# Kernel tuning notes

Hardware: AMD Instinct MI355X
Metric: run time of the kernel (lower is better)

## Reference

```python
import jax, jax.numpy as jnp
import numpy as np

HDIM = 1024
CDIM = 256
TEMPER = 10.0
IGNORE_OUT = 0.0
EPS = 1e-6


def setup_inputs() -> dict:
    key = jax.random.key(0)
    ks = jax.random.split(key, 6)
    B, T, D = 2, 128, 384
    x = jax.random.normal(ks[0], (B, T, D), jnp.float32)
    y = jax.random.normal(ks[1], (B, T, D), jnp.float32)
    # xavier-normal style init for the two linear layers
    W_enc = jax.random.normal(ks[2], (D, HDIM), jnp.float32) * np.sqrt(2.0 / (D + HDIM))
    b_enc = jnp.zeros((HDIM,), jnp.float32)
    W_dec = jax.random.normal(ks[3], (HDIM, D), jnp.float32) * np.sqrt(2.0 / (D + HDIM))
    b_dec = jnp.zeros((D,), jnp.float32)
    return {"x": x, "y": y, "W_enc": W_enc, "b_enc": b_enc, "W_dec": W_dec, "b_dec": b_dec}


def reference(x, y, W_enc, b_enc, W_dec, b_dec):
    B, T, D = x.shape
    n_iter = HDIM // CDIM
    pad = D - 1
    # shift_idx[s, j] = s + j : window of width D at offset s, s in [0, 2D-2]
    shift_idx = jnp.arange(2 * D - 1)[:, None] + jnp.arange(D)[None, :]

    seq_mask = (y == IGNORE_OUT)                       # (B,T,D) bool
    denom_seq = jnp.sum(~seq_mask).astype(x.dtype)
    qn = jnp.linalg.norm(y, axis=-1)                   # (B,T)

    mask_prev = None
    x_dis, losses = [], []
    for _ in range(n_iter):
        # --- _pad_for_shift: (B,T,2D-1,D) shifted windows of x ---
        kp = jnp.pad(x, ((0, 0), (0, 0), (pad, pad)))  # (B,T,3D-2)
        kpt = kp[..., shift_idx]                       # (B,T,2D-1,D)
        # --- _score (cos) + argmax over shifts ---
        kn = jnp.linalg.norm(kpt, axis=-1)             # (B,T,2D-1)
        sim = jnp.einsum('btsd,btd->bts', kpt, y) / (qn[..., None] * kn + EPS)
        sim = jnp.where(jnp.isnan(sim), 0.0, sim)
        theta = jnp.argmax(sim, axis=-1)               # (B,T) int
        x_opt = jnp.take_along_axis(kpt, theta[..., None, None], axis=-2)[..., 0, :]  # (B,T,D)
        # --- attention: elementwise cos-scaled score, temp softmax, detached ---
        dn = (jnp.linalg.norm(x_opt, axis=-1, keepdims=True)
              * jnp.linalg.norm(y, axis=-1, keepdims=True) + EPS)
        attn = jax.nn.softmax((x_opt * y / dn) / TEMPER, axis=-1)
        attn = jnp.where(jnp.isnan(attn), 0.0, attn)
        attn = jax.lax.stop_gradient(attn)
        x_attn = x_opt * attn
        # --- _reverse_pad_for_shift: window at offset 2D-2-theta ---
        kp2 = jnp.pad(x_attn, ((0, 0), (0, 0), (pad, pad)))
        rev_idx = (2 * D - 2 - theta)[..., None] + jnp.arange(D)  # (B,T,D)
        x_ele = jnp.take_along_axis(kp2, rev_idx, axis=-1)         # (B,T,D)
        # --- self_net: encoder -> top-k sparsify -> decoder_self ---
        h = x_ele @ W_enc + b_enc                      # (B,T,HDIM)
        if mask_prev is not None:
            h = jnp.where(mask_prev > 0, 1e-10, h)
        _, idx_top = jax.lax.top_k(h, CDIM)            # (B,T,CDIM)
        flat = idx_top.reshape(B * T, CDIM)
        mask_cur = jnp.zeros((B * T, HDIM), x.dtype).at[
            jnp.arange(B * T)[:, None], flat].set(1.0).reshape(B, T, HDIM)
        if mask_prev is None:
            mask_prev = mask_cur
        else:
            mask_prev = mask_prev + mask_cur - mask_prev * mask_cur
        h = h * mask_cur
        out = h @ W_dec + b_dec                        # (B,T,D)
        x_dis.append(out)
        # --- SeqLoss (masked MSE, mean-reduced by count of valid elems) ---
        err = jnp.where(seq_mask, 0.0, (out - x) ** 2) / denom_seq
        losses.append(jnp.sum(err))
    return jnp.stack(x_dis), jnp.stack(losses)
```

## Files before the change

### kernel.cpp

```cpp
#include <hip/hip_runtime.h>
#include <math.h>

#define DD 384
#define HD 1024
#define CD 256
#define NS 765
#define NITER 4
#define NROWS 256
#define TEMPER_F 10.0f
#define EPSF 1e-6f
#define CUTF 1e-10f

typedef unsigned long long u64;
typedef unsigned int u32;

__device__ __forceinline__ u32 flipf(float f) {
    u32 u = __float_as_uint(f);
    return u ^ ((u32)((int)u >> 31) | 0x80000000u);
}
__device__ __forceinline__ float unflipf(u32 s) {
    u32 fl = ~s;
    u32 u = (fl & 0x80000000u) ? (fl ^ 0x80000000u) : ~fl;
    return __uint_as_float(u);
}
__device__ __forceinline__ u64 shflx64(u64 v, int m) {
    int lo = __shfl_xor((int)(u32)v, m, 64);
    int hi = __shfl_xor((int)(u32)(v >> 32), m, 64);
    return ((u64)(u32)hi << 32) | (u32)lo;
}

__global__ __launch_bounds__(512) void fused_kernel(
    const float* __restrict__ x, const float* __restrict__ y,
    const float* __restrict__ Wenc, const float* __restrict__ benc,
    const float* __restrict__ Wdec, const float* __restrict__ bdec,
    float* __restrict__ out_xdis, float* __restrict__ lossp,
    int* __restrict__ ycnt)
{
    const int row  = blockIdx.x;
    const int tid  = threadIdx.x;
    const int lane = tid & 63;
    const int wid  = tid >> 6;

    __shared__ __align__(16) float xpad[1152];
    __shared__ __align__(16) float yr[DD];
    __shared__ float xa[DD];
    __shared__ __align__(16) float xe_s[DD];
    __shared__ __align__(16) float hpart[HD];
    __shared__ __align__(16) u64   skey[HD];
    __shared__ __align__(16) uint2 dec2[HD];
    __shared__ float wred[8];
    __shared__ int   wredi[8];
    __shared__ float wredn[8];
    __shared__ float s_sc[4];
    __shared__ int   s_theta, s_fb;
    __shared__ float loss4[NITER];

    const float* xrow = x + row * DD;
    const float* yrow = y + row * DD;

    for (int i = tid; i < 1152; i += 512)
        xpad[i] = (i >= DD - 1 && i < 2 * DD - 1) ? xrow[i - (DD - 1)] : 0.f;
    if (tid < DD) yr[tid] = yrow[tid];
    __syncthreads();

    if (tid < DD) {
        float p = yr[tid] * yr[tid];
        for (int o = 32; o; o >>= 1) p += __shfl_xor(p, o, 64);
        if (lane == 0) wred[wid] = p;
    }
    __syncthreads();
    if (tid == 0) {
        float s = 0.f;
        for (int w = 0; w < 6; ++w) s += wred[w];
        s_sc[0] = sqrtf(s);
    }
    __syncthreads();
    const float qn = s_sc[0];

    float bv = -INFINITY; int bs = 0x7fffffff; float bn = 0.f;
    if (tid < 192) {
        const float4* xp4 = (const float4*)xpad;
        const float4* yp4 = (const float4*)yr;
        float4 A = xp4[tid];
        const float f0 = A.x * A.x, f1 = A.y * A.y, f2 = A.z * A.z;
        float d0 = 0.f, d1 = 0.f, d2 = 0.f, d3 = 0.f, n0 = 0.f;
#pragma unroll 4
        for (int jc = 0; jc < 96; ++jc) {
            float4 B = xp4[tid + jc + 1];
            float4 Y = yp4[jc];
            d0 += A.x * Y.x; d0 += A.y * Y.y; d0 += A.z * Y.z; d0 += A.w * Y.w;
            d1 += A.y * Y.x; d1 += A.z * Y.y; d1 += A.w * Y.z; d1 += B.x * Y.w;
            d2 += A.z * Y.x; d2 += A.w * Y.y; d2 += B.x * Y.z; d2 += B.y * Y.w;
            d3 += A.w * Y.x; d3 += B.x * Y.y; d3 += B.y * Y.z; d3 += B.z * Y.w;
            n0 += A.x * A.x; n0 += A.y * A.y; n0 += A.z * A.z; n0 += A.w * A.w;
            A = B;
        }
        const float n1 = n0 - f0 + A.x * A.x;
        const float n2 = n1 - f1 + A.y * A.y;
        const float n3 = n2 - f2 + A.z * A.z;
        const int s0 = 4 * tid;
        float sim0 = d0 / (qn * sqrtf(n0) + EPSF);
        float sim1 = d1 / (qn * sqrtf(n1) + EPSF);
        float sim2 = d2 / (qn * sqrtf(n2) + EPSF);
        float sim3 = d3 / (qn * sqrtf(n3) + EPSF);
        bv = sim0; bs = s0; bn = n0;
        if (s0 + 1 < NS && sim1 > bv) { bv = sim1; bs = s0 + 1; bn = n1; }
        if (s0 + 2 < NS && sim2 > bv) { bv = sim2; bs = s0 + 2; bn = n2; }
        if (s0 + 3 < NS && sim3 > bv) { bv = sim3; bs = s0 + 3; bn = n3; }
    }
    for (int o = 32; o; o >>= 1) {
        float v2 = __shfl_xor(bv, o, 64);
        int   i2 = __shfl_xor(bs, o, 64);
        float n2 = __shfl_xor(bn, o, 64);
        if (v2 > bv || (v2 == bv && i2 < bs)) { bv = v2; bs = i2; bn = n2; }
    }
    if (lane == 0) { wred[wid] = bv; wredi[wid] = bs; wredn[wid] = bn; }
    __syncthreads();
    if (tid == 0) {
        float v = wred[0]; int b = wredi[0]; float nn = wredn[0];
        for (int w = 1; w < 8; ++w)
            if (wred[w] > v || (wred[w] == v && wredi[w] < b)) {
                v = wred[w]; b = wredi[w]; nn = wredn[w];
            }
        s_theta = b;
        s_sc[1] = sqrtf(nn) * qn + EPSF;
    }
    __syncthreads();
    const int theta = s_theta;
    const float dn = s_sc[1];

    float xo = 0.f, z = 0.f;
    if (tid < DD) {
        xo = xpad[theta + tid];
        z = (xo * yr[tid] / dn) / TEMPER_F;
        float m = z;
        for (int o = 32; o; o >>= 1) { float w2 = __shfl_xor(m, o, 64); if (w2 > m) m = w2; }
        if (lane == 0) wred[wid] = m;
    }
    __syncthreads();
    if (tid == 0) {
        float m = wred[0];
        for (int w = 1; w < 6; ++w) if (wred[w] > m) m = wred[w];
        s_sc[2] = m;
    }
    __syncthreads();
    float ez = 0.f;
    if (tid < DD) {
        ez = expf(z - s_sc[2]);
        float p = ez;
        for (int o = 32; o; o >>= 1) p += __shfl_xor(p, o, 64);
        if (lane == 0) wred[wid] = p;
    }
    __syncthreads();
    if (tid == 0) {
        float s = 0.f;
        for (int w = 0; w < 6; ++w) s += wred[w];
        s_sc[3] = s;
    }
    __syncthreads();
    if (tid < DD) {
        xa[tid] = xo * (ez / s_sc[3]);
        int c = (yr[tid] != 0.f) ? 1 : 0;
        for (int o = 32; o; o >>= 1) c += __shfl_xor(c, o, 64);
        if (lane == 0) wredi[wid] = c;
    }
    __syncthreads();
    if (tid == 0) {
        int s = 0;
        for (int w = 0; w < 6; ++w) s += wredi[w];
        ycnt[row] = s;
    }
    if (tid < DD) {
        int sj = tid - (theta - (DD - 1));
        xe_s[tid] = (sj >= 0 && sj < DD) ? xa[sj] : 0.f;
    }
    __syncthreads();

    const int c4 = tid & 255;
    const int jh = tid >> 8;
    float4 acc = make_float4(0.f, 0.f, 0.f, 0.f);
    {
        const float* wbase = Wenc + (size_t)(jh * 192) * HD + 4 * c4;
        const float* xb = xe_s + jh * 192;
#pragma unroll 8
        for (int j = 0; j < 192; ++j) {
            float xv = xb[j];
            float4 w = *(const float4*)(wbase + (size_t)j * HD);
            acc.x += xv * w.x; acc.y += xv * w.y;
            acc.z += xv * w.z; acc.w += xv * w.w;
        }
    }
    if (jh == 1) *(float4*)&hpart[4 * c4] = acc;
    if (tid == 0) s_fb = HD;
    if (tid < NITER) loss4[tid] = 0.f;
    __syncthreads();
    if (jh == 0) {
        float4 hp = *(const float4*)&hpart[4 * c4];
        float4 bb = *(const float4*)&benc[4 * c4];
        float hv0 = acc.x + hp.x + bb.x;
        float hv1 = acc.y + hp.y + bb.y;
        float hv2 = acc.z + hp.z + bb.z;
        float hv3 = acc.w + hp.w + bb.w;
        const int col = 4 * c4;
        skey[col + 0] = ((u64)(~flipf(hv0)) << 32) | (u32)(col + 0);
        skey[col + 1] = ((u64)(~flipf(hv1)) << 32) | (u32)(col + 1);
        skey[col + 2] = ((u64)(~flipf(hv2)) << 32) | (u32)(col + 2);
        skey[col + 3] = ((u64)(~flipf(hv3)) << 32) | (u32)(col + 3);
    }
    __syncthreads();

    u64 e0 = skey[2 * tid];
    u64 e1 = skey[2 * tid + 1];
    for (int k = 2; k <= HD; k <<= 1) {
        const bool up = ((2 * tid) & k) == 0;
        for (int j = k >> 1; j > 0; j >>= 1) {
            if (j == 1) {
                bool sw = up ? (e0 > e1) : (e0 < e1);
                if (sw) { u64 t2 = e0; e0 = e1; e1 = t2; }
            } else if (j <= 64) {
                const int m = j >> 1;
                u64 p0 = shflx64(e0, m);
                u64 p1 = shflx64(e1, m);
                const bool takeMin = (((tid & m) == 0) == up);
                e0 = takeMin ? (e0 < p0 ? e0 : p0) : (e0 > p0 ? e0 : p0);
                e1 = takeMin ? (e1 < p1 ? e1 : p1) : (e1 > p1 ? e1 : p1);
            } else {
                __syncthreads();
                skey[2 * tid]     = e0;
                skey[2 * tid + 1] = e1;
                __syncthreads();
                const int tp = tid ^ (j >> 1);
                u64 p0 = skey[2 * tp];
                u64 p1 = skey[2 * tp + 1];
                const bool takeMin = (((tid & (j >> 1)) == 0) == up);
                e0 = takeMin ? (e0 < p0 ? e0 : p0) : (e0 > p0 ? e0 : p0);
                e1 = takeMin ? (e1 < p1 ? e1 : p1) : (e1 > p1 ? e1 : p1);
            }
        }
    }

    {
        float v0 = unflipf((u32)(e0 >> 32));
        float v1 = unflipf((u32)(e1 >> 32));
        dec2[2 * tid]     = make_uint2(__float_as_uint(v0), ((u32)e0) * DD);
        dec2[2 * tid + 1] = make_uint2(__float_as_uint(v1), ((u32)e1) * DD);
        int fbloc = HD;
        if (!(v1 > CUTF)) fbloc = 2 * tid + 1;
        if (!(v0 > CUTF)) fbloc = 2 * tid;
        for (int o = 32; o; o >>= 1) { int t2 = __shfl_xor(fbloc, o, 64); if (t2 < fbloc) fbloc = t2; }
        if (lane == 0) atomicMin(&s_fb, fbloc);
    }
    __syncthreads();
    const int fb = s_fb;

    {
        const int k = tid >> 7;
        const int g = tid & 127;
        const bool active = (g < 96);
        int n = 0;
        if (active) {
            n = (k == 0) ? CD : fb - k * CD;
            if (n < 0) n = 0; if (n > CD) n = CD;
        }
        float4 oacc = make_float4(0.f, 0.f, 0.f, 0.f);
        if (active) oacc = *(const float4*)&bdec[4 * g];
        const float* wd = Wdec + 4 * g;
        const int base = k * CD;
        int r = 0;
        for (; r + 2 <= n; r += 2) {
            uint4 dv = *(const uint4*)&dec2[base + r];
            float v0 = __uint_as_float(dv.x);
            float4 w0 = *(const float4*)(wd + dv.y);
            float v1 = __uint_as_float(dv.z);
            float4 w1 = *(const float4*)(wd + dv.w);
            oacc.x += v0 * w0.x; oacc.y += v0 * w0.y;
            oacc.z += v0 * w0.z; oacc.w += v0 * w0.w;
            oacc.x += v1 * w1.x; oacc.y += v1 * w1.y;
            oacc.z += v1 * w1.z; oacc.w += v1 * w1.w;
        }
        if (r < n) {
            uint2 dv = dec2[base + r];
            float v0 = __uint_as_float(dv.x);
            float4 w0 = *(const float4*)(wd + dv.y);
            oacc.x += v0 * w0.x; oacc.y += v0 * w0.y;
            oacc.z += v0 * w0.z; oacc.w += v0 * w0.w;
        }
        float l = 0.f;
        if (active) {
            *(float4*)&out_xdis[((size_t)k * NROWS + row) * DD + 4 * g] = oacc;
            float4 xv = *(const float4*)&xrow[4 * g];
            float4 yv = *(const float4*)&yr[4 * g];
            float e;
            e = oacc.x - xv.x; if (yv.x != 0.f) l += e * e;
            e = oacc.y - xv.y; if (yv.y != 0.f) l += e * e;
            e = oacc.z - xv.z; if (yv.z != 0.f) l += e * e;
            e = oacc.w - xv.w; if (yv.w != 0.f) l += e * e;
        }
        for (int o = 32; o; o >>= 1) l += __shfl_xor(l, o, 64);
        if (lane == 0) atomicAdd(&loss4[k], l);
    }
    __syncthreads();
    if (tid < NITER) lossp[row * NITER + tid] = loss4[tid];
}

__global__ __launch_bounds__(256) void finalize2(
    const float* __restrict__ lossp, const int* __restrict__ ycnt,
    float* __restrict__ losses)
{
    const int tid = threadIdx.x, lane = tid & 63, w = tid >> 6;
    __shared__ int ctot[4];
    int c = ycnt[tid];
    for (int o = 32; o; o >>= 1) c += __shfl_xor(c, o, 64);
    if (lane == 0) ctot[w] = c;
    __syncthreads();
    const int total = ctot[0] + ctot[1] + ctot[2] + ctot[3];
    float s = lossp[lane * NITER + w] + lossp[(lane + 64) * NITER + w]
            + lossp[(lane + 128) * NITER + w] + lossp[(lane + 192) * NITER + w];
    for (int o = 32; o; o >>= 1) s += __shfl_xor(s, o, 64);
    if (lane == 0) losses[w] = s / (float)total;
}

extern "C" void kernel_launch(void* const* d_in, const int* in_sizes, int n_in,
                              void* d_out, int out_size, void* d_ws, size_t ws_size,
                              hipStream_t stream) {
    const float* x    = (const float*)d_in[0];
    const float* y    = (const float*)d_in[1];
    const float* Wenc = (const float*)d_in[2];
    const float* benc = (const float*)d_in[3];
    const float* Wdec = (const float*)d_in[4];
    const float* bdec = (const float*)d_in[5];

    float* out  = (float*)d_out;
    float* loss = out + (out_size - NITER);

    float* lossp = (float*)d_ws;
    int*   ycnt  = (int*)(lossp + NROWS * NITER);

    fused_kernel<<<NROWS, 512, 0, stream>>>(x, y, Wenc, benc, Wdec, bdec,
                                            out, lossp, ycnt);
    finalize2<<<1, 256, 0, stream>>>(lossp, ycnt, loss);
}
```

Before: 113.5 us.

## Split fused per-row kernel into prep, tiled encoder GEMM, sort, and decoder kernels

Breaks the single per-row fused kernel into four stages that pass data through global workspace: shift/attention prep, an encoder GEMM, a per-row bitonic sort, and a decoder. The encoder GEMM tiles 8 rows per block, so each Wenc load is reused across 8 rows instead of being reread by every row block. The decoder now runs one block per (row, iteration) with 4-way split-K, which gives more parallelism. The cost is extra kernel launches and global round-trips for xe, h and the sorted value/offset arrays.

```diff
diff --git a/kernel.cpp b/kernel.cpp
--- a/kernel.cpp
+++ b/kernel.cpp
@@ -29,12 +29,9 @@
     return ((u64)(u32)hi << 32) | (u32)lo;
 }
 
-__global__ __launch_bounds__(512) void fused_kernel(
+__global__ __launch_bounds__(512) void prep_kernel(
     const float* __restrict__ x, const float* __restrict__ y,
-    const float* __restrict__ Wenc, const float* __restrict__ benc,
-    const float* __restrict__ Wdec, const float* __restrict__ bdec,
-    float* __restrict__ out_xdis, float* __restrict__ lossp,
-    int* __restrict__ ycnt)
+    float* __restrict__ xe_g, int* __restrict__ ycnt)
 {
     const int row  = blockIdx.x;
     const int tid  = threadIdx.x;
@@ -44,16 +41,11 @@
     __shared__ __align__(16) float xpad[1152];
     __shared__ __align__(16) float yr[DD];
     __shared__ float xa[DD];
-    __shared__ __align__(16) float xe_s[DD];
-    __shared__ __align__(16) float hpart[HD];
-    __shared__ __align__(16) u64   skey[HD];
-    __shared__ __align__(16) uint2 dec2[HD];
     __shared__ float wred[8];
     __shared__ int   wredi[8];
     __shared__ float wredn[8];
     __shared__ float s_sc[4];
-    __shared__ int   s_theta, s_fb;
-    __shared__ float loss4[NITER];
+    __shared__ int   s_theta;
 
     const float* xrow = x + row * DD;
     const float* yrow = y + row * DD;
@@ -172,45 +164,60 @@
     }
     if (tid < DD) {
         int sj = tid - (theta - (DD - 1));
-        xe_s[tid] = (sj >= 0 && sj < DD) ? xa[sj] : 0.f;
-    }
-    __syncthreads();
-
-    const int c4 = tid & 255;
-    const int jh = tid >> 8;
+        xe_g[row * DD + tid] = (sj >= 0 && sj < DD) ? xa[sj] : 0.f;
+    }
+}
+
+__global__ __launch_bounds__(256) void enc_gemm(
+    const float* __restrict__ xe_g, const float* __restrict__ Wenc,
+    const float* __restrict__ benc, float* __restrict__ h_g)
+{
+    const int rt = blockIdx.x >> 3;
+    const int ct = blockIdx.x & 7;
+    const int tid = threadIdx.x;
+    __shared__ __align__(16) float A[8 * DD];
+    {
+        const float4* src = (const float4*)(xe_g + (size_t)rt * 8 * DD);
+        float4* dst = (float4*)A;
+        for (int i = tid; i < 8 * DD / 4; i += 256) dst[i] = src[i];
+    }
+    __syncthreads();
+    const int r  = tid >> 5;
+    const int c4 = (tid & 31) << 2;
+    const int col = ct * 128 + c4;
+    const float* wp = Wenc + col;
+    const float* ar = A + r * DD;
     float4 acc = make_float4(0.f, 0.f, 0.f, 0.f);
-    {
-        const float* wbase = Wenc + (size_t)(jh * 192) * HD + 4 * c4;
-        const float* xb = xe_s + jh * 192;
-#pragma unroll 8
-        for (int j = 0; j < 192; ++j) {
-            float xv = xb[j];
-            float4 w = *(const float4*)(wbase + (size_t)j * HD);
-            acc.x += xv * w.x; acc.y += xv * w.y;
-            acc.z += xv * w.z; acc.w += xv * w.w;
-        }
-    }
-    if (jh == 1) *(float4*)&hpart[4 * c4] = acc;
+#pragma unroll 4
+    for (int j = 0; j < DD; ++j) {
+        float a = ar[j];
+        float4 w = *(const float4*)(wp + (size_t)j * HD);
+        acc.x += a * w.x; acc.y += a * w.y;
+        acc.z += a * w.z; acc.w += a * w.w;
+    }
+    float4 bb = *(const float4*)(benc + col);
+    acc.x += bb.x; acc.y += bb.y; acc.z += bb.z; acc.w += bb.w;
+    *(float4*)(h_g + (size_t)(rt * 8 + r) * HD + col) = acc;
+}
+
+__global__ __launch_bounds__(512) void sort_kernel(
+    const float* __restrict__ h_g, uint2* __restrict__ svo_g,
+    int* __restrict__ fbs)
+{
+    const int row  = blockIdx.x;
+    const int tid  = threadIdx.x;
+    const int lane = tid & 63;
+
+    __shared__ __align__(16) u64 skey[HD];
+    __shared__ int s_fb;
+
+    const float* hrow = h_g + (size_t)row * HD;
+    float2 hh = *(const float2*)(hrow + 2 * tid);
+    u64 e0 = ((u64)(~flipf(hh.x)) << 32) | (u32)(2 * tid);
+    u64 e1 = ((u64)(~flipf(hh.y)) << 32) | (u32)(2 * tid + 1);
     if (tid == 0) s_fb = HD;
-    if (tid < NITER) loss4[tid] = 0.f;
-    __syncthreads();
-    if (jh == 0) {
-        float4 hp = *(const float4*)&hpart[4 * c4];
-        float4 bb = *(const float4*)&benc[4 * c4];
-        float hv0 = acc.x + hp.x + bb.x;
-        float hv1 = acc.y + hp.y + bb.y;
-        float hv2 = acc.z + hp.z + bb.z;
-        float hv3 = acc.w + hp.w + bb.w;
-        const int col = 4 * c4;
-        skey[col + 0] = ((u64)(~flipf(hv0)) << 32) | (u32)(col + 0);
-        skey[col + 1] = ((u64)(~flipf(hv1)) << 32) | (u32)(col + 1);
-        skey[col + 2] = ((u64)(~flipf(hv2)) << 32) | (u32)(col + 2);
-        skey[col + 3] = ((u64)(~flipf(hv3)) << 32) | (u32)(col + 3);
-    }
-    __syncthreads();
-
-    u64 e0 = skey[2 * tid];
-    u64 e1 = skey[2 * tid + 1];
+    __syncthreads();
+
     for (int k = 2; k <= HD; k <<= 1) {
         const bool up = ((2 * tid) & k) == 0;
         for (int j = k >> 1; j > 0; j >>= 1) {
@@ -242,8 +249,8 @@
     {
         float v0 = unflipf((u32)(e0 >> 32));
         float v1 = unflipf((u32)(e1 >> 32));
-        dec2[2 * tid]     = make_uint2(__float_as_uint(v0), ((u32)e0) * DD);
-        dec2[2 * tid + 1] = make_uint2(__float_as_uint(v1), ((u32)e1) * DD);
+        svo_g[row * HD + 2 * tid]     = make_uint2(__float_as_uint(v0), ((u32)e0) * DD);
+        svo_g[row * HD + 2 * tid + 1] = make_uint2(__float_as_uint(v1), ((u32)e1) * DD);
         int fbloc = HD;
         if (!(v1 > CUTF)) fbloc = 2 * tid + 1;
         if (!(v0 > CUTF)) fbloc = 2 * tid;
@@ -251,56 +258,83 @@
         if (lane == 0) atomicMin(&s_fb, fbloc);
     }
     __syncthreads();
-    const int fb = s_fb;
-
-    {
-        const int k = tid >> 7;
-        const int g = tid & 127;
-        const bool active = (g < 96);
-        int n = 0;
-        if (active) {
-            n = (k == 0) ? CD : fb - k * CD;
-            if (n < 0) n = 0; if (n > CD) n = CD;
+    if (tid == 0) fbs[row] = s_fb;
+}
+
+__global__ __launch_bounds__(384) void dec_kernel(
+    const uint2* __restrict__ svo_g, const int* __restrict__ fbs,
+    const float* __restrict__ Wdec, const float* __restrict__ bdec,
+    const float* __restrict__ x, const float* __restrict__ y,
+    float* __restrict__ out_xdis, float* __restrict__ lossp)
+{
+    const int row = blockIdx.x >> 2;
+    const int k   = blockIdx.x & 3;
+    const int tid = threadIdx.x;
+    const int lane = tid & 63;
+    const int wid  = tid >> 6;
+    const int grp = tid / 96;
+    const int t   = tid - grp * 96;
+
+    __shared__ __align__(16) uint2 vo[CD];
+    __shared__ __align__(16) float part[3][DD];
+    __shared__ float wred[6];
+
+    if (tid < CD) vo[tid] = svo_g[(size_t)row * HD + k * CD + tid];
+    __syncthreads();
+    const int fb = fbs[row];
+    int n = (k == 0) ? CD : fb - k * CD;
+    if (n < 0) n = 0; if (n > CD) n = CD;
+
+    const float* wd = Wdec + 4 * t;
+    float4 acc = make_float4(0.f, 0.f, 0.f, 0.f);
+    int r = grp;
+    for (; r + 13 <= n; r += 16) {
+#pragma unroll
+        for (int q = 0; q < 4; ++q) {
+            uint2 dv = vo[r + 4 * q];
+            float v = __uint_as_float(dv.x);
+            float4 w = *(const float4*)(wd + dv.y);
+            acc.x += v * w.x; acc.y += v * w.y;
+            acc.z += v * w.z; acc.w += v * w.w;
         }
-        float4 oacc = make_float4(0.f, 0.f, 0.f, 0.f);
-        if (active) oacc = *(const float4*)&bdec[4 * g];
-        const float* wd = Wdec + 4 * g;
-        const int base = k * CD;
-        int r = 0;
-        for (; r + 2 <= n; r += 2) {
-            uint4 dv = *(const uint4*)&dec2[base + r];
-            float v0 = __uint_as_float(dv.x);
-            float4 w0 = *(const float4*)(wd + dv.y);
-            float v1 = __uint_as_float(dv.z);
-            float4 w1 = *(const float4*)(wd + dv.w);
-            oacc.x += v0 * w0.x; oacc.y += v0 * w0.y;
-            oacc.z += v0 * w0.z; oacc.w += v0 * w0.w;
-            oacc.x += v1 * w1.x; oacc.y += v1 * w1.y;
-            oacc.z += v1 * w1.z; oacc.w += v1 * w1.w;
-        }
-        if (r < n) {
-            uint2 dv = dec2[base + r];
-            float v0 = __uint_as_float(dv.x);
-            float4 w0 = *(const float4*)(wd + dv.y);
-            oacc.x += v0 * w0.x; oacc.y += v0 * w0.y;
-            oacc.z += v0 * w0.z; oacc.w += v0 * w0.w;
-        }
-        float l = 0.f;
-        if (active) {
-            *(float4*)&out_xdis[((size_t)k * NROWS + row) * DD + 4 * g] = oacc;
-            float4 xv = *(const float4*)&xrow[4 * g];
-            float4 yv = *(const float4*)&yr[4 * g];
-            float e;
-            e = oacc.x - xv.x; if (yv.x != 0.f) l += e * e;
-            e = oacc.y - xv.y; if (yv.y != 0.f) l += e * e;
-            e = oacc.z - xv.z; if (yv.z != 0.f) l += e * e;
-            e = oacc.w - xv.w; if (yv.w != 0.f) l += e * e;
-        }
-        for (int o = 32; o; o >>= 1) l += __shfl_xor(l, o, 64);
-        if (lane == 0) atomicAdd(&loss4[k], l);
-    }
-    __syncthreads();
-    if (tid < NITER) lossp[row * NITER + tid] = loss4[tid];
+    }
+    for (; r < n; r += 4) {
+        uint2 dv = vo[r];
+        float v = __uint_as_float(dv.x);
+        float4 w = *(const float4*)(wd + dv.y);
+        acc.x += v * w.x; acc.y += v * w.y;
+        acc.z += v * w.z; acc.w += v * w.w;
+    }
+    if (grp) *(float4*)&part[grp - 1][4 * t] = acc;
+    __syncthreads();
+
+    float l = 0.f;
+    if (grp == 0) {
+        float4 p1 = *(const float4*)&part[0][4 * t];
+        float4 p2 = *(const float4*)&part[1][4 * t];
+        float4 p3 = *(const float4*)&part[2][4 * t];
+        float4 bb = *(const float4*)&bdec[4 * t];
+        acc.x += p1.x + p2.x + p3.x + bb.x;
+        acc.y += p1.y + p2.y + p3.y + bb.y;
+        acc.z += p1.z + p2.z + p3.z + bb.z;
+        acc.w += p1.w + p2.w + p3.w + bb.w;
+        *(float4*)&out_xdis[((size_t)k * NROWS + row) * DD + 4 * t] = acc;
+        float4 xv = *(const float4*)&x[row * DD + 4 * t];
+        float4 yv = *(const float4*)&y[row * DD + 4 * t];
+        float e;
+        e = acc.x - xv.x; if (yv.x != 0.f) l += e * e;
+        e = acc.y - xv.y; if (yv.y != 0.f) l += e * e;
+        e = acc.z - xv.z; if (yv.z != 0.f) l += e * e;
+        e = acc.w - xv.w; if (yv.w != 0.f) l += e * e;
+    }
+    for (int o = 32; o; o >>= 1) l += __shfl_xor(l, o, 64);
+    if (lane == 0) wred[wid] = l;
+    __syncthreads();
+    if (tid == 0) {
+        float s = 0.f;
+        for (int w = 0; w < 6; ++w) s += wred[w];
+        lossp[row * NITER + k] = s;
+    }
 }
 
 __global__ __launch_bounds__(256) void finalize2(
@@ -333,10 +367,17 @@
     float* out  = (float*)d_out;
     float* loss = out + (out_size - NITER);
 
-    float* lossp = (float*)d_ws;
-    int*   ycnt  = (int*)(lossp + NROWS * NITER);
-
-    fused_kernel<<<NROWS, 512, 0, stream>>>(x, y, Wenc, benc, Wdec, bdec,
-                                            out, lossp, ycnt);
+    int*   ycnt  = (int*)d_ws;
+    float* lossp = (float*)(ycnt + NROWS);
+    float* xe_g  = lossp + NROWS * NITER;
+    float* h_g   = xe_g + (size_t)NROWS * DD;
+    uint2* svo_g = (uint2*)(h_g + (size_t)NROWS * HD);
+    int*   fbs   = (int*)(svo_g + (size_t)NROWS * HD);
+
+    prep_kernel<<<NROWS, 512, 0, stream>>>(x, y, xe_g, ycnt);
+    enc_gemm<<<256, 256, 0, stream>>>(xe_g, Wenc, benc, h_g);
+    sort_kernel<<<NROWS, 512, 0, stream>>>(h_g, svo_g, fbs);
+    dec_kernel<<<NROWS * NITER, 384, 0, stream>>>(svo_g, fbs, Wdec, bdec,
+                                                  x, y, out, lossp);
     finalize2<<<1, 256, 0, stream>>>(lossp, ycnt, loss);
 }
```

Measured after the change: 146.3 us. 28.8% more time.
